# Optimization experiments

Measured on AMD Instinct MI355X. Metric: run time of the kernel, lower is better.

Reference implementation:

```python
import jax, jax.numpy as jnp
import numpy as np

N_NODES = 50000
N_EDGES = 800000
HID = 128


def setup_inputs() -> dict:
    key = jax.random.key(0)
    k = jax.random.split(key, 8)
    nfeats = jax.random.normal(k[0], (N_NODES, HID), dtype=jnp.float32)
    efeats = jax.random.normal(k[1], (N_EDGES, HID), dtype=jnp.float32)
    src = jax.random.randint(k[2], (N_EDGES,), 0, N_NODES, dtype=jnp.int32)
    dst = jax.random.randint(k[3], (N_EDGES,), 0, N_NODES, dtype=jnp.int32)
    # eW: Linear(3H -> H); nW: Linear(2H -> H) (torch Linear: x @ W.T + b)
    We = jax.random.normal(k[4], (3 * HID, HID), dtype=jnp.float32) / np.sqrt(3 * HID)
    be = jnp.zeros((HID,), dtype=jnp.float32)
    Wn = jax.random.normal(k[5], (2 * HID, HID), dtype=jnp.float32) / np.sqrt(2 * HID)
    bn = jnp.zeros((HID,), dtype=jnp.float32)
    return {"nfeats": nfeats, "efeats": efeats, "src": src, "dst": dst,
            "We": We, "be": be, "Wn": Wn, "bn": bn}


def reference(nfeats, efeats, src, dst, We, be, Wn, bn):
    # --- edge message: m = ReLU(Linear(cat[src_nh, eh, dst_nh]))
    eh = jnp.concatenate([nfeats[src], efeats, nfeats[dst]], axis=-1)  # [E, 3H]
    m = jax.nn.relu(eh @ We + be)  # [E, H]
    # --- mean-reduce messages to destination nodes (DGL fn.mean: 0 for isolated nodes)
    summed = jax.ops.segment_sum(m, dst, num_segments=N_NODES)  # [N, H]
    cnt = jax.ops.segment_sum(jnp.ones((m.shape[0],), m.dtype), dst, num_segments=N_NODES)
    h = summed / jnp.maximum(cnt, 1.0)[:, None]  # [N, H]
    # --- node update: h = ReLU(Linear(cat[nh, h]))
    nh = jnp.concatenate([nfeats, h], axis=-1)  # [N, 2H]
    h_out = jax.nn.relu(nh @ Wn + bn)  # [N, H]
    # --- residuals
    return h_out + nfeats, m + efeats
```

## Files before the change

kernel.cpp:

```cpp
#include <hip/hip_runtime.h>
#include <stdint.h>

#define N_NODES 50000
#define N_EDGES 800000
#define HID 128

typedef __attribute__((ext_vector_type(8))) short bf16x8;
typedef __attribute__((ext_vector_type(4))) float f32x4;

__device__ inline uint32_t pack_bf16(float x, float y) {
    uint32_t a = __builtin_bit_cast(uint32_t, x) + 0x8000u;
    uint32_t b = __builtin_bit_cast(uint32_t, y) + 0x8000u;
    return (b & 0xffff0000u) | (a >> 16);
}

__device__ inline unsigned short cvt_bf16(float x) {
    return (unsigned short)((__builtin_bit_cast(uint32_t, x) + 0x8000u) >> 16);
}

__device__ inline bf16x8 load_row8_bf16(const float* p) {
    const float4* q = (const float4*)p;
    float4 u = q[0], v = q[1];
    union { bf16x8 v8; uint32_t u32[4]; } r;
    r.u32[0] = pack_bf16(u.x, u.y);
    r.u32[1] = pack_bf16(u.z, u.w);
    r.u32[2] = pack_bf16(v.x, v.y);
    r.u32[3] = pack_bf16(v.z, v.w);
    return r.v8;
}

__device__ inline void gload16(const float* g, float* l) {
    __builtin_amdgcn_global_load_lds(
        (const __attribute__((address_space(1))) void*)g,
        (__attribute__((address_space(3))) void*)l, 16, 0, 0);
}

__device__ inline float lds_ef_read(const float* ef, int row, int n) {
    return ef[row * 128 + ((((n >> 2) ^ (row & 7)) << 2) | (n & 3))];
}

__device__ inline bf16x8 load_frag_lds(const float* ef, int row, int c16) {
    int s = row & 7;
    float4 u = *(const float4*)(ef + row * 128 + ((c16 ^ s) << 2));
    float4 v = *(const float4*)(ef + row * 128 + (((c16 + 1) ^ s) << 2));
    union { bf16x8 v8; uint32_t u32[4]; } r;
    r.u32[0] = pack_bf16(u.x, u.y);
    r.u32[1] = pack_bf16(u.z, u.w);
    r.u32[2] = pack_bf16(v.x, v.y);
    r.u32[3] = pack_bf16(v.z, v.w);
    return r.v8;
}

#define WE_SHUF_ELEMS (12 * 8 * 64 * 8)
#define WN_SHUF_ELEMS (8 * 8 * 64 * 8)
__global__ void prep_kernel(const float* __restrict__ We, const float* __restrict__ Wn,
                            unsigned short* __restrict__ We_shuf,
                            unsigned short* __restrict__ Wn_shuf) {
    int tid = blockIdx.x * blockDim.x + threadIdx.x;
    if (tid < WE_SHUF_ELEMS) {
        int j = tid & 7, lane = (tid >> 3) & 63, tt = tid >> 9;
        int t = tt & 7, kk = tt >> 3;
        int k = kk * 32 + (lane >> 4) * 8 + j;
        int n = t * 16 + (lane & 15);
        We_shuf[tid] = cvt_bf16(We[k * HID + n]);
    } else if (tid < WE_SHUF_ELEMS + WN_SHUF_ELEMS) {
        int id = tid - WE_SHUF_ELEMS;
        int j = id & 7, lane = (id >> 3) & 63, tt = id >> 9;
        int t = tt & 7, kk = tt >> 3;
        int k = kk * 32 + (lane >> 4) * 8 + j;
        int n = t * 16 + (lane & 15);
        Wn_shuf[id] = cvt_bf16(Wn[k * HID + n]);
    }
}

__global__ void hist_kernel(const int* __restrict__ dst, int* __restrict__ bend) {
    int e = blockIdx.x * blockDim.x + threadIdx.x;
    if (e < N_EDGES) atomicAdd(&bend[dst[e]], 1);
}

#define SCAN_T 1024
__global__ __launch_bounds__(1024) void scan_kernel(int* __restrict__ bend) {
    __shared__ int part[SCAN_T];
    int t = threadIdx.x;
    const int chunk = (N_NODES + SCAN_T - 1) / SCAN_T;
    int lo = t * chunk;
    int hi = lo + chunk;
    if (hi > N_NODES) hi = N_NODES;
    if (lo > N_NODES) lo = N_NODES;
    int s = 0;
    for (int i = lo; i < hi; ++i) s += bend[i];
    part[t] = s;
    __syncthreads();
    for (int off = 1; off < SCAN_T; off <<= 1) {
        int v = 0;
        if (t >= off) v = part[t - off];
        __syncthreads();
        if (t >= off) part[t] += v;
        __syncthreads();
    }
    int excl = (t == 0) ? 0 : part[t - 1];
    for (int i = lo; i < hi; ++i) {
        int v = bend[i];
        bend[i] = excl;
        excl += v;
    }
}

__global__ void scatter_kernel(const int* __restrict__ dst, int* __restrict__ bend,
                               int* __restrict__ order, int* __restrict__ rank) {
    int e = blockIdx.x * blockDim.x + threadIdx.x;
    if (e < N_EDGES) {
        int pos = atomicAdd(&bend[dst[e]], 1);
        order[pos] = e;
        rank[e] = pos;
    }
}

__global__ __launch_bounds__(128) void edge_kernel(
    const float* __restrict__ nfeats, const float* __restrict__ efeats,
    const int* __restrict__ src, const int* __restrict__ dst,
    const unsigned short* __restrict__ We_shuf, const float* __restrict__ be,
    float* __restrict__ out1, float* __restrict__ msorted, const int* __restrict__ rank) {
    __shared__ float ef_lds[2][32 * 128];
    int w = threadIdx.x >> 6;
    int wid = blockIdx.x * 2 + w;
    int lane = threadIdx.x & 63;
    int e0 = wid * 32;
    int m = lane & 15, quad = lane >> 4;
    float* ef = &ef_lds[w][0];

#pragma unroll
    for (int i = 0; i < 16; ++i) {
        int row = 2 * i + (lane >> 5);
        int c16 = (lane & 31) ^ (row & 7);
        gload16(efeats + (size_t)(e0 + row) * HID + c16 * 4, ef + i * 256);
    }

    int r0 = e0 + m, r1 = e0 + 16 + m;
    const float* s0 = nfeats + (size_t)src[r0] * HID;
    const float* s1 = nfeats + (size_t)src[r1] * HID;
    const float* d0 = nfeats + (size_t)dst[r0] * HID;
    const float* d1 = nfeats + (size_t)dst[r1] * HID;

    f32x4 acc[2][8];
#pragma unroll
    for (int mi = 0; mi < 2; ++mi)
#pragma unroll
        for (int t = 0; t < 8; ++t) acc[mi][t] = (f32x4){0.f, 0.f, 0.f, 0.f};

    const bf16x8* W = (const bf16x8*)We_shuf;

#pragma unroll
    for (int kk = 0; kk < 4; ++kk) {
        int off = kk * 32 + quad * 8;
        bf16x8 a0 = load_row8_bf16(s0 + off);
        bf16x8 a1 = load_row8_bf16(s1 + off);
#pragma unroll
        for (int t = 0; t < 8; ++t) {
            bf16x8 b = W[(kk * 8 + t) * 64 + lane];
            acc[0][t] = __builtin_amdgcn_mfma_f32_16x16x32_bf16(a0, b, acc[0][t], 0, 0, 0);
            acc[1][t] = __builtin_amdgcn_mfma_f32_16x16x32_bf16(a1, b, acc[1][t], 0, 0, 0);
        }
    }
#pragma unroll
    for (int kk = 8; kk < 12; ++kk) {
        int off = (kk - 8) * 32 + quad * 8;
        bf16x8 a0 = load_row8_bf16(d0 + off);
        bf16x8 a1 = load_row8_bf16(d1 + off);
#pragma unroll
        for (int t = 0; t < 8; ++t) {
            bf16x8 b = W[(kk * 8 + t) * 64 + lane];
            acc[0][t] = __builtin_amdgcn_mfma_f32_16x16x32_bf16(a0, b, acc[0][t], 0, 0, 0);
            acc[1][t] = __builtin_amdgcn_mfma_f32_16x16x32_bf16(a1, b, acc[1][t], 0, 0, 0);
        }
    }

    asm volatile("s_waitcnt vmcnt(0)" ::: "memory");

#pragma unroll
    for (int kk = 4; kk < 8; ++kk) {
        int c16 = (kk - 4) * 8 + quad * 2;
        bf16x8 a0 = load_frag_lds(ef, m, c16);
        bf16x8 a1 = load_frag_lds(ef, 16 + m, c16);
#pragma unroll
        for (int t = 0; t < 8; ++t) {
            bf16x8 b = W[(kk * 8 + t) * 64 + lane];
            acc[0][t] = __builtin_amdgcn_mfma_f32_16x16x32_bf16(a0, b, acc[0][t], 0, 0, 0);
            acc[1][t] = __builtin_amdgcn_mfma_f32_16x16x32_bf16(a1, b, acc[1][t], 0, 0, 0);
        }
    }

    float bev[8];
#pragma unroll
    for (int t = 0; t < 8; ++t) bev[t] = be[t * 16 + m];

    if (msorted) {
#pragma unroll
        for (int mi = 0; mi < 2; ++mi) {
#pragma unroll
            for (int r = 0; r < 4; ++r) {
                int lrow = mi * 16 + quad * 4 + r;
                int e = e0 + lrow;
                float* o = out1 + (size_t)e * HID;
                float* ms = msorted + (size_t)rank[e] * HID;
#pragma unroll
                for (int t = 0; t < 8; ++t) {
                    int n = t * 16 + m;
                    float v = fmaxf(acc[mi][t][r] + bev[t], 0.0f);
                    o[n] = v + lds_ef_read(ef, lrow, n);
                    ms[n] = v;
                }
            }
        }
    } else {
#pragma unroll
        for (int mi = 0; mi < 2; ++mi) {
#pragma unroll
            for (int r = 0; r < 4; ++r) {
                int lrow = mi * 16 + quad * 4 + r;
                int e = e0 + lrow;
                float* o = out1 + (size_t)e * HID;
#pragma unroll
                for (int t = 0; t < 8; ++t) {
                    int n = t * 16 + m;
                    float v = fmaxf(acc[mi][t][r] + bev[t], 0.0f);
                    o[n] = v + lds_ef_read(ef, lrow, n);
                }
            }
        }
    }
}

__global__ __launch_bounds__(256) void gather_sorted(
    const float* __restrict__ msorted, const int* __restrict__ bend,
    float* __restrict__ h) {
    int wid = blockIdx.x * 4 + (threadIdx.x >> 6);
    if (wid >= N_NODES) return;
    int lane = threadIdx.x & 63;
    int start = (wid == 0) ? 0 : bend[wid - 1];
    int end = bend[wid];
    const float2* base = (const float2*)msorted;
    float ax = 0.f, ay = 0.f;
    int j = start;
    for (; j + 4 <= end; j += 4) {
        float2 v0 = base[(size_t)(j + 0) * 64 + lane];
        float2 v1 = base[(size_t)(j + 1) * 64 + lane];
        float2 v2 = base[(size_t)(j + 2) * 64 + lane];
        float2 v3 = base[(size_t)(j + 3) * 64 + lane];
        ax += (v0.x + v1.x) + (v2.x + v3.x);
        ay += (v0.y + v1.y) + (v2.y + v3.y);
    }
    for (; j < end; ++j) {
        float2 v = base[(size_t)j * 64 + lane];
        ax += v.x;
        ay += v.y;
    }
    int deg = end - start;
    float inv = (deg > 0) ? 1.0f / (float)deg : 0.0f;
    float2 r;
    r.x = ax * inv;
    r.y = ay * inv;
    ((float2*)(h + (size_t)wid * HID))[lane] = r;
}

__global__ __launch_bounds__(256) void gather_kernel(
    const float* __restrict__ out1, const float* __restrict__ efeats,
    const int* __restrict__ order, const int* __restrict__ bend,
    float* __restrict__ h) {
    int wid = blockIdx.x * 4 + (threadIdx.x >> 6);
    if (wid >= N_NODES) return;
    int lane = threadIdx.x & 63;
    int start = (wid == 0) ? 0 : bend[wid - 1];
    int end = bend[wid];
    float ax = 0.0f, ay = 0.0f;
    int j = start;
    for (; j + 2 <= end; j += 2) {
        int ea = order[j], eb = order[j + 1];
        float2 o1 = ((const float2*)(out1 + (size_t)ea * HID))[lane];
        float2 f1 = ((const float2*)(efeats + (size_t)ea * HID))[lane];
        float2 o2 = ((const float2*)(out1 + (size_t)eb * HID))[lane];
        float2 f2 = ((const float2*)(efeats + (size_t)eb * HID))[lane];
        ax += (o1.x - f1.x) + (o2.x - f2.x);
        ay += (o1.y - f1.y) + (o2.y - f2.y);
    }
    if (j < end) {
        int ea = order[j];
        float2 o1 = ((const float2*)(out1 + (size_t)ea * HID))[lane];
        float2 f1 = ((const float2*)(efeats + (size_t)ea * HID))[lane];
        ax += o1.x - f1.x;
        ay += o1.y - f1.y;
    }
    int deg = end - start;
    float inv = (deg > 0) ? 1.0f / (float)deg : 0.0f;
    float2 r;
    r.x = ax * inv;
    r.y = ay * inv;
    ((float2*)(h + (size_t)wid * HID))[lane] = r;
}

__global__ __launch_bounds__(256) void node_kernel(
    const float* __restrict__ nfeats, const unsigned short* __restrict__ Wn_shuf,
    const float* __restrict__ bn, const float* __restrict__ h,
    float* __restrict__ out0) {
    int wid = blockIdx.x * 4 + (threadIdx.x >> 6);
    int n0 = wid * 16;
    if (n0 >= N_NODES) return;
    int lane = threadIdx.x & 63;
    int m = lane & 15, quad = lane >> 4;
    int row = n0 + m;
    const float* pn = nfeats + (size_t)row * HID;
    const float* ph = h + (size_t)row * HID;

    f32x4 acc[8];
#pragma unroll
    for (int t = 0; t < 8; ++t) acc[t] = (f32x4){0.f, 0.f, 0.f, 0.f};

    const bf16x8* W = (const bf16x8*)Wn_shuf;

#pragma unroll
    for (int kk = 0; kk < 8; ++kk) {
        int k = kk * 32 + quad * 8;
        bf16x8 a = (k < 128) ? load_row8_bf16(pn + k)
                             : load_row8_bf16(ph + (k - 128));
#pragma unroll
        for (int t = 0; t < 8; ++t) {
            bf16x8 b = W[(kk * 8 + t) * 64 + lane];
            acc[t] = __builtin_amdgcn_mfma_f32_16x16x32_bf16(a, b, acc[t], 0, 0, 0);
        }
    }

    float bnv[8];
#pragma unroll
    for (int t = 0; t < 8; ++t) bnv[t] = bn[t * 16 + m];

#pragma unroll
    for (int r = 0; r < 4; ++r) {
        int rw = n0 + quad * 4 + r;
        const float* nf = nfeats + (size_t)rw * HID;
        float* o = out0 + (size_t)rw * HID;
#pragma unroll
        for (int t = 0; t < 8; ++t) {
            int n = t * 16 + m;
            float v = fmaxf(acc[t][r] + bnv[t], 0.0f);
            o[n] = v + nf[n];
        }
    }
}

extern "C" void kernel_launch(void* const* d_in, const int* in_sizes, int n_in,
                              void* d_out, int out_size, void* d_ws, size_t ws_size,
                              hipStream_t stream) {
    const float* nfeats = (const float*)d_in[0];
    const float* efeats = (const float*)d_in[1];
    const int* src = (const int*)d_in[2];
    const int* dst = (const int*)d_in[3];
    const float* We = (const float*)d_in[4];
    const float* be = (const float*)d_in[5];
    const float* Wn = (const float*)d_in[6];
    const float* bn = (const float*)d_in[7];

    float* out0 = (float*)d_out;
    float* out1 = out0 + (size_t)N_NODES * HID;

    int* rank = (int*)d_out;
    int* order = rank + N_EDGES;
    int* bend = order + N_EDGES;

    float* h = (float*)d_ws;
    unsigned short* We_shuf = (unsigned short*)(h + (size_t)N_NODES * HID);
    unsigned short* Wn_shuf = We_shuf + WE_SHUF_ELEMS;
    size_t base_bytes = (size_t)N_NODES * HID * 4 + (size_t)(WE_SHUF_ELEMS + WN_SHUF_ELEMS) * 2;
    size_t need = base_bytes + (size_t)N_EDGES * HID * 4;
    float* msorted = (ws_size >= need) ? (float*)((char*)d_ws + base_bytes) : nullptr;

    hipMemsetAsync(bend, 0, N_NODES * sizeof(int), stream);

    prep_kernel<<<(WE_SHUF_ELEMS + WN_SHUF_ELEMS) / 256, 256, 0, stream>>>(We, Wn, We_shuf, Wn_shuf);

    hist_kernel<<<N_EDGES / 256, 256, 0, stream>>>(dst, bend);
    scan_kernel<<<1, SCAN_T, 0, stream>>>(bend);
    scatter_kernel<<<N_EDGES / 256, 256, 0, stream>>>(dst, bend, order, rank);

    edge_kernel<<<12500, 128, 0, stream>>>(nfeats, efeats, src, dst, We_shuf, be,
                                           out1, msorted, rank);

    if (msorted) {
        gather_sorted<<<12500, 256, 0, stream>>>(msorted, bend, h);
    } else {
        gather_kernel<<<12500, 256, 0, stream>>>(out1, efeats, order, bend, h);
    }

    node_kernel<<<782, 256, 0, stream>>>(nfeats, Wn_shuf, bn, h, out0);
}
```

Baseline: 1.248 ms.

## Fuse mean aggregation into edge kernel via dst-sorted segmented atomics

The edge kernel now processes edges in dst-sorted order through the `order` permutation. Each wave reduces its messages per destination segment with shuffles and atomically adds the partial sums into a zeroed node-sum buffer. This removes the large sorted-message buffer write, the separate gather kernel and the rank array, and the node kernel applies the 1/deg scaling when it loads the sums. In exchange, efeats and out1 rows are accessed in permuted (gathered/scattered) order, float atomics make summation order nondeterministic, and a larger memset is needed to zero the sums.

```diff
diff --git a/kernel.cpp b/kernel.cpp
--- a/kernel.cpp
+++ b/kernel.cpp
@@ -26,6 +26,17 @@
     r.u32[1] = pack_bf16(u.z, u.w);
     r.u32[2] = pack_bf16(v.x, v.y);
     r.u32[3] = pack_bf16(v.z, v.w);
+    return r.v8;
+}
+
+__device__ inline bf16x8 load_row8_bf16_scaled(const float* p, float s) {
+    const float4* q = (const float4*)p;
+    float4 u = q[0], v = q[1];
+    union { bf16x8 v8; uint32_t u32[4]; } r;
+    r.u32[0] = pack_bf16(u.x * s, u.y * s);
+    r.u32[1] = pack_bf16(u.z * s, u.w * s);
+    r.u32[2] = pack_bf16(v.x * s, v.y * s);
+    r.u32[3] = pack_bf16(v.z * s, v.w * s);
     return r.v8;
 }
 
@@ -107,20 +118,20 @@
 }
 
 __global__ void scatter_kernel(const int* __restrict__ dst, int* __restrict__ bend,
-                               int* __restrict__ order, int* __restrict__ rank) {
+                               int* __restrict__ order) {
     int e = blockIdx.x * blockDim.x + threadIdx.x;
     if (e < N_EDGES) {
         int pos = atomicAdd(&bend[dst[e]], 1);
         order[pos] = e;
-        rank[e] = pos;
     }
 }
 
 __global__ __launch_bounds__(128) void edge_kernel(
     const float* __restrict__ nfeats, const float* __restrict__ efeats,
     const int* __restrict__ src, const int* __restrict__ dst,
+    const int* __restrict__ order,
     const unsigned short* __restrict__ We_shuf, const float* __restrict__ be,
-    float* __restrict__ out1, float* __restrict__ msorted, const int* __restrict__ rank) {
+    float* __restrict__ out1, float* __restrict__ sums) {
     __shared__ float ef_lds[2][32 * 128];
     int w = threadIdx.x >> 6;
     int wid = blockIdx.x * 2 + w;
@@ -129,18 +140,27 @@
     int m = lane & 15, quad = lane >> 4;
     float* ef = &ef_lds[w][0];
 
-#pragma unroll
-    for (int i = 0; i < 16; ++i) {
-        int row = 2 * i + (lane >> 5);
+    int i = lane;
+    int e_i = 0, d_i = 0;
+    if (i < 32) {
+        e_i = order[e0 + i];
+        d_i = dst[e_i];
+    }
+
+#pragma unroll
+    for (int it = 0; it < 16; ++it) {
+        int row = 2 * it + (lane >> 5);
+        int er = __shfl(e_i, row);
         int c16 = (lane & 31) ^ (row & 7);
-        gload16(efeats + (size_t)(e0 + row) * HID + c16 * 4, ef + i * 256);
-    }
-
-    int r0 = e0 + m, r1 = e0 + 16 + m;
-    const float* s0 = nfeats + (size_t)src[r0] * HID;
-    const float* s1 = nfeats + (size_t)src[r1] * HID;
-    const float* d0 = nfeats + (size_t)dst[r0] * HID;
-    const float* d1 = nfeats + (size_t)dst[r1] * HID;
+        gload16(efeats + (size_t)er * HID + c16 * 4, ef + it * 256);
+    }
+
+    int ea = __shfl(e_i, m), eb = __shfl(e_i, 16 + m);
+    int da = __shfl(d_i, m), db = __shfl(d_i, 16 + m);
+    const float* s0 = nfeats + (size_t)src[ea] * HID;
+    const float* s1 = nfeats + (size_t)src[eb] * HID;
+    const float* d0 = nfeats + (size_t)da * HID;
+    const float* d1 = nfeats + (size_t)db * HID;
 
     f32x4 acc[2][8];
 #pragma unroll
@@ -194,122 +214,73 @@
 #pragma unroll
     for (int t = 0; t < 8; ++t) bev[t] = be[t * 16 + m];
 
-    if (msorted) {
+#pragma unroll
+    for (int mi = 0; mi < 2; ++mi) {
+#pragma unroll
+        for (int r = 0; r < 4; ++r) {
+            int lrow = mi * 16 + quad * 4 + r;
+            int e = __shfl(e_i, lrow);
+            float* o = out1 + (size_t)e * HID;
+#pragma unroll
+            for (int t = 0; t < 8; ++t) {
+                int n = t * 16 + m;
+                float v = fmaxf(acc[mi][t][r] + bev[t], 0.0f);
+                acc[mi][t][r] = v;
+                o[n] = v + lds_ef_read(ef, lrow, n);
+            }
+        }
+    }
+
+    int dprev = __shfl(d_i, (i == 0) ? 0 : i - 1);
+    bool head = (i < 32) && (i == 0 || d_i != dprev);
+    unsigned long long mask = __ballot(head);
+    while (mask) {
+        int a = __builtin_ctzll(mask);
+        mask &= mask - 1;
+        int b = mask ? __builtin_ctzll(mask) : 32;
+        int nd = __shfl(d_i, a);
+        float tot[8];
+#pragma unroll
+        for (int t = 0; t < 8; ++t) tot[t] = 0.f;
 #pragma unroll
         for (int mi = 0; mi < 2; ++mi) {
 #pragma unroll
             for (int r = 0; r < 4; ++r) {
                 int lrow = mi * 16 + quad * 4 + r;
-                int e = e0 + lrow;
-                float* o = out1 + (size_t)e * HID;
-                float* ms = msorted + (size_t)rank[e] * HID;
-#pragma unroll
-                for (int t = 0; t < 8; ++t) {
-                    int n = t * 16 + m;
-                    float v = fmaxf(acc[mi][t][r] + bev[t], 0.0f);
-                    o[n] = v + lds_ef_read(ef, lrow, n);
-                    ms[n] = v;
-                }
+                bool in = (lrow >= a) && (lrow < b);
+#pragma unroll
+                for (int t = 0; t < 8; ++t) tot[t] += in ? acc[mi][t][r] : 0.0f;
             }
         }
-    } else {
-#pragma unroll
-        for (int mi = 0; mi < 2; ++mi) {
-#pragma unroll
-            for (int r = 0; r < 4; ++r) {
-                int lrow = mi * 16 + quad * 4 + r;
-                int e = e0 + lrow;
-                float* o = out1 + (size_t)e * HID;
-#pragma unroll
-                for (int t = 0; t < 8; ++t) {
-                    int n = t * 16 + m;
-                    float v = fmaxf(acc[mi][t][r] + bev[t], 0.0f);
-                    o[n] = v + lds_ef_read(ef, lrow, n);
-                }
-            }
-        }
-    }
-}
-
-__global__ __launch_bounds__(256) void gather_sorted(
-    const float* __restrict__ msorted, const int* __restrict__ bend,
-    float* __restrict__ h) {
-    int wid = blockIdx.x * 4 + (threadIdx.x >> 6);
-    if (wid >= N_NODES) return;
-    int lane = threadIdx.x & 63;
-    int start = (wid == 0) ? 0 : bend[wid - 1];
-    int end = bend[wid];
-    const float2* base = (const float2*)msorted;
-    float ax = 0.f, ay = 0.f;
-    int j = start;
-    for (; j + 4 <= end; j += 4) {
-        float2 v0 = base[(size_t)(j + 0) * 64 + lane];
-        float2 v1 = base[(size_t)(j + 1) * 64 + lane];
-        float2 v2 = base[(size_t)(j + 2) * 64 + lane];
-        float2 v3 = base[(size_t)(j + 3) * 64 + lane];
-        ax += (v0.x + v1.x) + (v2.x + v3.x);
-        ay += (v0.y + v1.y) + (v2.y + v3.y);
-    }
-    for (; j < end; ++j) {
-        float2 v = base[(size_t)j * 64 + lane];
-        ax += v.x;
-        ay += v.y;
-    }
-    int deg = end - start;
-    float inv = (deg > 0) ? 1.0f / (float)deg : 0.0f;
-    float2 r;
-    r.x = ax * inv;
-    r.y = ay * inv;
-    ((float2*)(h + (size_t)wid * HID))[lane] = r;
-}
-
-__global__ __launch_bounds__(256) void gather_kernel(
-    const float* __restrict__ out1, const float* __restrict__ efeats,
-    const int* __restrict__ order, const int* __restrict__ bend,
-    float* __restrict__ h) {
-    int wid = blockIdx.x * 4 + (threadIdx.x >> 6);
-    if (wid >= N_NODES) return;
-    int lane = threadIdx.x & 63;
-    int start = (wid == 0) ? 0 : bend[wid - 1];
-    int end = bend[wid];
-    float ax = 0.0f, ay = 0.0f;
-    int j = start;
-    for (; j + 2 <= end; j += 2) {
-        int ea = order[j], eb = order[j + 1];
-        float2 o1 = ((const float2*)(out1 + (size_t)ea * HID))[lane];
-        float2 f1 = ((const float2*)(efeats + (size_t)ea * HID))[lane];
-        float2 o2 = ((const float2*)(out1 + (size_t)eb * HID))[lane];
-        float2 f2 = ((const float2*)(efeats + (size_t)eb * HID))[lane];
-        ax += (o1.x - f1.x) + (o2.x - f2.x);
-        ay += (o1.y - f1.y) + (o2.y - f2.y);
-    }
-    if (j < end) {
-        int ea = order[j];
-        float2 o1 = ((const float2*)(out1 + (size_t)ea * HID))[lane];
-        float2 f1 = ((const float2*)(efeats + (size_t)ea * HID))[lane];
-        ax += o1.x - f1.x;
-        ay += o1.y - f1.y;
-    }
-    int deg = end - start;
-    float inv = (deg > 0) ? 1.0f / (float)deg : 0.0f;
-    float2 r;
-    r.x = ax * inv;
-    r.y = ay * inv;
-    ((float2*)(h + (size_t)wid * HID))[lane] = r;
+#pragma unroll
+        for (int t = 0; t < 8; ++t) {
+            tot[t] += __shfl_xor(tot[t], 16);
+            tot[t] += __shfl_xor(tot[t], 32);
+        }
+        float* srow = sums + (size_t)nd * HID;
+#pragma unroll
+        for (int q = 0; q < 2; ++q) {
+            int t = quad + q * 4;
+            atomicAdd(&srow[t * 16 + m], tot[t]);
+        }
+    }
 }
 
 __global__ __launch_bounds__(256) void node_kernel(
     const float* __restrict__ nfeats, const unsigned short* __restrict__ Wn_shuf,
-    const float* __restrict__ bn, const float* __restrict__ h,
-    float* __restrict__ out0) {
+    const float* __restrict__ bn, const float* __restrict__ sums,
+    const int* __restrict__ bend, float* __restrict__ out0) {
     int wid = blockIdx.x * 4 + (threadIdx.x >> 6);
     int n0 = wid * 16;
     if (n0 >= N_NODES) return;
     int lane = threadIdx.x & 63;
     int m = lane & 15, quad = lane >> 4;
     int row = n0 + m;
+    int end = bend[row];
+    int start = (row == 0) ? 0 : bend[row - 1];
+    float inv = 1.0f / fmaxf((float)(end - start), 1.0f);
     const float* pn = nfeats + (size_t)row * HID;
-    const float* ph = h + (size_t)row * HID;
+    const float* ps = sums + (size_t)row * HID;
 
     f32x4 acc[8];
 #pragma unroll
@@ -321,7 +292,7 @@
     for (int kk = 0; kk < 8; ++kk) {
         int k = kk * 32 + quad * 8;
         bf16x8 a = (k < 128) ? load_row8_bf16(pn + k)
-                             : load_row8_bf16(ph + (k - 128));
+                             : load_row8_bf16_scaled(ps + (k - 128), inv);
 #pragma unroll
         for (int t = 0; t < 8; ++t) {
             bf16x8 b = W[(kk * 8 + t) * 64 + lane];
@@ -362,33 +333,26 @@
     float* out0 = (float*)d_out;
     float* out1 = out0 + (size_t)N_NODES * HID;
 
-    int* rank = (int*)d_out;
-    int* order = rank + N_EDGES;
-    int* bend = order + N_EDGES;
-
-    float* h = (float*)d_ws;
-    unsigned short* We_shuf = (unsigned short*)(h + (size_t)N_NODES * HID);
+    int* order = (int*)d_out;
+
+    float* sums = (float*)d_ws;
+    unsigned short* We_shuf = (unsigned short*)(sums + (size_t)N_NODES * HID);
     unsigned short* Wn_shuf = We_shuf + WE_SHUF_ELEMS;
-    size_t base_bytes = (size_t)N_NODES * HID * 4 + (size_t)(WE_SHUF_ELEMS + WN_SHUF_ELEMS) * 2;
-    size_t need = base_bytes + (size_t)N_EDGES * HID * 4;
-    float* msorted = (ws_size >= need) ? (float*)((char*)d_ws + base_bytes) : nullptr;
-
-    hipMemsetAsync(bend, 0, N_NODES * sizeof(int), stream);
+    int* bend = (int*)(Wn_shuf + WN_SHUF_ELEMS);
+
+    hipMemsetAsync(d_ws, 0,
+                   (size_t)N_NODES * HID * 4 + (WE_SHUF_ELEMS + WN_SHUF_ELEMS) * 2 +
+                       N_NODES * sizeof(int),
+                   stream);
 
     prep_kernel<<<(WE_SHUF_ELEMS + WN_SHUF_ELEMS) / 256, 256, 0, stream>>>(We, Wn, We_shuf, Wn_shuf);
 
     hist_kernel<<<N_EDGES / 256, 256, 0, stream>>>(dst, bend);
     scan_kernel<<<1, SCAN_T, 0, stream>>>(bend);
-    scatter_kernel<<<N_EDGES / 256, 256, 0, stream>>>(dst, bend, order, rank);
-
-    edge_kernel<<<12500, 128, 0, stream>>>(nfeats, efeats, src, dst, We_shuf, be,
-                                           out1, msorted, rank);
-
-    if (msorted) {
-        gather_sorted<<<12500, 256, 0, stream>>>(msorted, bend, h);
-    } else {
-        gather_kernel<<<12500, 256, 0, stream>>>(out1, efeats, order, bend, h);
-    }
-
-    node_kernel<<<782, 256, 0, stream>>>(nfeats, Wn_shuf, bn, h, out0);
-}
+    scatter_kernel<<<N_EDGES / 256, 256, 0, stream>>>(dst, bend, order);
+
+    edge_kernel<<<12500, 128, 0, stream>>>(nfeats, efeats, src, dst, order,
+                                           We_shuf, be, out1, sums);
+
+    node_kernel<<<782, 256, 0, stream>>>(nfeats, Wn_shuf, bn, sums, bend, out0);
+}
```

New measurement: 1.073 ms. 1.16x faster.
